# Kernel tuning notes

Hardware: AMD Instinct MI355X
Metric: run time of the kernel (lower is better)

## Reference

```python
import jax, jax.numpy as jnp
import numpy as np

N_EMBD = 1024
N_HEAD = 16
R = 16
SCALING = 1.0 / 16.0  # loralib default lora_alpha=1, scaling = alpha/r


def lora_linear(x, W, b, A, B):
    # loralib: y = x @ W.T + b + (x @ A.T) @ B.T * scaling
    return x @ W.T + b + (x @ A.T) @ B.T * SCALING


def setup_inputs() -> dict:
    key = jax.random.key(0)
    ks = jax.random.split(key, 16)
    B, T, S, C = 8, 1024, 256, N_EMBD
    std = 0.02
    return {
        "x": jax.random.normal(ks[0], (B, T, C), jnp.float32),
        "feature": jax.random.normal(ks[1], (B, S, C), jnp.float32),
        # c_attn (q projection)
        "Wq": jax.random.normal(ks[2], (C, C), jnp.float32) * std,
        "bq": jnp.zeros((C,), jnp.float32),
        "Aq": jax.random.normal(ks[3], (R, C), jnp.float32) * std,
        "Bq": jnp.zeros((C, R), jnp.float32),
        # feature_attn (kv projection)
        "Wf": jax.random.normal(ks[4], (2 * C, C), jnp.float32) * std,
        "bf": jnp.zeros((2 * C,), jnp.float32),
        "Af": jax.random.normal(ks[5], (R, C), jnp.float32) * std,
        "Bf": jnp.zeros((2 * C, R), jnp.float32),
        # c_proj
        "Wp": jax.random.normal(ks[6], (C, C), jnp.float32) * std,
        "bp": jnp.zeros((C,), jnp.float32),
        "Ap": jax.random.normal(ks[7], (R, C), jnp.float32) * std,
        "Bp": jnp.zeros((C, R), jnp.float32),
    }


def reference(x, feature, Wq, bq, Aq, Bq, Wf, bf, Af, Bf, Wp, bp, Ap, Bp):
    Bsz, T, C = x.shape
    S = feature.shape[1]
    H = N_HEAD
    D = C // H

    q = lora_linear(x, Wq, bq, Aq, Bq).reshape(Bsz, T, H, D).transpose(0, 2, 1, 3)
    kv = lora_linear(feature, Wf, bf, Af, Bf)
    k, v = kv[..., :C], kv[..., C:]
    k = k.reshape(Bsz, S, H, D).transpose(0, 2, 1, 3)
    v = v.reshape(Bsz, S, H, D).transpose(0, 2, 1, 3)

    att = jnp.einsum("bhtd,bhsd->bhts", q, k) * (1.0 / np.sqrt(D))
    mask = jnp.tril(jnp.ones((T, S), bool))  # bias[:, :, :T, :S]
    att = jnp.where(mask, att, -jnp.inf)
    att = jax.nn.softmax(att, axis=-1)

    y = jnp.einsum("bhts,bhsd->bhtd", att, v)
    y = y.transpose(0, 2, 1, 3).reshape(Bsz, T, C)
    return lora_linear(y, Wp, bp, Ap, Bp)
```

## Files before the change

### kernel.cpp

```cpp
#include <hip/hip_runtime.h>
#include <hip/hip_bf16.h>
#include <stdint.h>
#include <stddef.h>

typedef __hip_bfloat16 bf16;
typedef __attribute__((ext_vector_type(8))) short short8;
typedef __attribute__((ext_vector_type(4))) float floatx4;

__device__ __forceinline__ void async_load16(const bf16* g, bf16* l) {
#if defined(__has_builtin) && __has_builtin(__builtin_amdgcn_global_load_lds)
  __builtin_amdgcn_global_load_lds((__attribute__((address_space(1))) void*)g,
                                   (__attribute__((address_space(3))) void*)l,
                                   16, 0, 0);
#else
  *(short8*)l = *(const short8*)g;
#endif
}

__device__ __forceinline__ int wave_detect_f32(const unsigned short* __restrict__ xr) {
  const int lane = threadIdx.x & 63;
  const unsigned short u = xr[lane];
  const int e = (u >> 7) & 0xFF;
  const unsigned long long m = __ballot(e >= 0x93);
  return (__popcll(m) > 5) ? 1 : 0;
}

__device__ __forceinline__ float ldf(const void* p, int i, int flg) {
  return flg ? ((const float*)p)[i] : __bfloat162float(((const bf16*)p)[i]);
}

struct PrepArgs {
  const void *x, *ft, *bq, *bf, *bp;
  const void *Wq, *Aq, *Bq, *Wf, *Af, *Bf, *Wp, *Ap, *Bp;
  bf16 *cx, *cft, *cbq, *cbf, *cbp, *weffq, *wefff, *weffp;
};

__device__ __forceinline__ void canon4(const void* src, bf16* dst, int i4, int flg) {
  if (flg) {
    const float4 v = ((const float4*)src)[i4];
    dst[i4 * 4 + 0] = __float2bfloat16(v.x);
    dst[i4 * 4 + 1] = __float2bfloat16(v.y);
    dst[i4 * 4 + 2] = __float2bfloat16(v.z);
    dst[i4 * 4 + 3] = __float2bfloat16(v.w);
  } else {
    ((uint2*)dst)[i4] = ((const uint2*)src)[i4];
  }
}

__device__ __forceinline__ void weff1(const void* W, const void* Bm, const void* Am,
                                      bf16* dst, int idx, int flg) {
  const int n = idx >> 10, k = idx & 1023;
  float acc = 0.f;
#pragma unroll
  for (int r = 0; r < 16; ++r)
    acc += ldf(Bm, n * 16 + r, flg) * ldf(Am, r * 1024 + k, flg);
  dst[idx] = __float2bfloat16(ldf(W, idx, flg) + 0.0625f * acc);
}

__global__ __launch_bounds__(256) void prep_kernel(PrepArgs a) {
  const int flg = wave_detect_f32((const unsigned short*)a.x);
  const int bid = blockIdx.x, tid = threadIdx.x;
  if (bid < 8192) {
    canon4(a.x, a.cx, bid * 256 + tid, flg);
  } else if (bid < 10240) {
    canon4(a.ft, a.cft, (bid - 8192) * 256 + tid, flg);
  } else if (bid < 10241) {
    canon4(a.bq, a.cbq, tid, flg);
  } else if (bid < 10243) {
    canon4(a.bf, a.cbf, (bid - 10241) * 256 + tid, flg);
  } else if (bid < 10244) {
    canon4(a.bp, a.cbp, tid, flg);
  } else if (bid < 14340) {
    weff1(a.Wq, a.Bq, a.Aq, a.weffq, (bid - 10244) * 256 + tid, flg);
  } else if (bid < 22532) {
    weff1(a.Wf, a.Bf, a.Af, a.wefff, (bid - 14340) * 256 + tid, flg);
  } else {
    weff1(a.Wp, a.Bp, a.Ap, a.weffp, (bid - 22532) * 256 + tid, flg);
  }
}

#define SLOT ((128 + 128) * 32)

__device__ __forceinline__ void stage_slot(const bf16* __restrict__ gA,
                                           const bf16* __restrict__ gB,
                                           bf16* slot, int tid) {
#pragma unroll
  for (int l = 0; l < 2; ++l) {
    const int D = l * 256 + tid;
    const int r = D >> 2;
    const int c = (D & 3) ^ ((r >> 1) & 3);
    async_load16(gA + (size_t)r * 1024 + c * 8, slot + D * 8);
  }
#pragma unroll
  for (int l = 0; l < 2; ++l) {
    const int D = l * 256 + tid;
    const int r = D >> 2;
    const int c = (D & 3) ^ ((r >> 1) & 3);
    async_load16(gB + (size_t)r * 1024 + c * 8, slot + 128 * 32 + D * 8);
  }
}

__device__ __forceinline__ void gemm_core(const bf16* __restrict__ A,
                                          const bf16* __restrict__ Bt,
                                          int bm, int bn, bf16* sT,
                                          floatx4 (&acc)[4][4]) {
  const int tid = threadIdx.x;
  const int wave = tid >> 6, lane = tid & 63;
  const int lrow = lane & 15, quad = lane >> 4;
  const int wm64 = (wave >> 1) << 6;
  const int wn64 = (wave & 1) << 6;
  const int pc0 = ((quad ^ ((lrow >> 1) & 3)) << 3);

  const bf16* gA = A + (size_t)bm * 1024;
  const bf16* gB = Bt + (size_t)bn * 1024;

  stage_slot(gA, gB, sT, tid);
  stage_slot(gA + 32, gB + 32, sT + SLOT, tid);

#pragma unroll
  for (int t = 0; t < 32; ++t) {
    asm volatile("s_waitcnt lgkmcnt(0)" ::: "memory");
    __builtin_amdgcn_s_barrier();
    __builtin_amdgcn_sched_barrier(0);
    if (t < 30) {
      stage_slot(gA + (t + 2) * 32, gB + (t + 2) * 32,
                 sT + ((t + 2) % 3) * SLOT, tid);
      asm volatile("s_waitcnt vmcnt(8)" ::: "memory");
    } else if (t == 30) {
      asm volatile("s_waitcnt vmcnt(4)" ::: "memory");
    } else {
      asm volatile("s_waitcnt vmcnt(0)" ::: "memory");
    }
    __builtin_amdgcn_s_barrier();
    __builtin_amdgcn_sched_barrier(0);

    const bf16* slotA = sT + (t % 3) * SLOT;
    const bf16* slotB = slotA + 128 * 32;
    short8 a_[4], b_[4];
#pragma unroll
    for (int i = 0; i < 4; ++i) {
      a_[i] = *(const short8*)(slotA + (wm64 + i * 16 + lrow) * 32 + pc0);
      b_[i] = *(const short8*)(slotB + (wn64 + i * 16 + lrow) * 32 + pc0);
    }
    __builtin_amdgcn_s_setprio(1);
#pragma unroll
    for (int i = 0; i < 4; ++i)
#pragma unroll
      for (int j = 0; j < 4; ++j)
        acc[i][j] = __builtin_amdgcn_mfma_f32_16x16x32_bf16(
            a_[i], b_[j], acc[i][j], 0, 0, 0);
    __builtin_amdgcn_s_setprio(0);
  }
}

__global__ __launch_bounds__(256, 3) void gemm_qkv(
    const bf16* __restrict__ cx, const bf16* __restrict__ cft,
    const bf16* __restrict__ weffq, const bf16* __restrict__ wefff,
    const bf16* __restrict__ cbq, const bf16* __restrict__ cbf,
    bf16* __restrict__ qws, bf16* __restrict__ kws, bf16* __restrict__ vtws) {
  __shared__ __align__(16) bf16 sT[3 * SLOT];
  const int bid = blockIdx.x;
  int mode, bm, bn;
  const bf16 *A, *Bt, *bias;
  if (bid < 512) {
    mode = 0; A = cx; Bt = weffq; bias = cbq;
    bm = (((bid & 7) << 3) | ((bid >> 3) & 7)) * 128;
    bn = (bid >> 6) * 128;
  } else {
    const int b2 = bid - 512;
    mode = 1; A = cft; Bt = wefff; bias = cbf;
    bm = (((b2 & 7) << 1) | ((b2 >> 3) & 1)) * 128;
    bn = (b2 >> 4) * 128;
  }

  const floatx4 zero4 = {0.f, 0.f, 0.f, 0.f};
  floatx4 acc[4][4];
#pragma unroll
  for (int i = 0; i < 4; ++i)
#pragma unroll
    for (int j = 0; j < 4; ++j) acc[i][j] = zero4;

  gemm_core(A, Bt, bm, bn, sT, acc);

  const int tid = threadIdx.x, wave = tid >> 6, lane = tid & 63;
  const int lrow = lane & 15, quad = lane >> 4;
  const int wm64 = (wave >> 1) << 6, wn64 = (wave & 1) << 6;
#pragma unroll
  for (int i = 0; i < 4; ++i) {
    const int mbase = bm + wm64 + i * 16 + quad * 4;
#pragma unroll
    for (int j = 0; j < 4; ++j) {
      const int n = bn + wn64 + j * 16 + lrow;
      const float bv = __bfloat162float(bias[n]);
#pragma unroll
      for (int r = 0; r < 4; ++r) {
        const int m = mbase + r;
        const bf16 hval = __float2bfloat16(acc[i][j][r] + bv);
        if (mode == 0) {
          const int b = m >> 10, t = m & 1023, hh = n >> 6, d = n & 63;
          qws[(((size_t)(b * 16 + hh)) * 1024 + t) * 64 + d] = hval;
        } else {
          const int b = m >> 8, s = m & 255;
          if (n < 1024) {
            const int hh = n >> 6, d = n & 63;
            kws[(((size_t)(b * 16 + hh)) * 256 + s) * 64 + d] = hval;
          } else {
            const int nn = n - 1024, hh = nn >> 6, d = nn & 63;
            vtws[(((size_t)(b * 16 + hh)) * 64 + d) * 256 + s] = hval;
          }
        }
      }
    }
  }
}

__global__ __launch_bounds__(256, 3) void gemm_out(
    const bf16* __restrict__ A, const bf16* __restrict__ Bt,
    const bf16* __restrict__ bias, void* __restrict__ out0,
    const unsigned short* __restrict__ xraw) {
  __shared__ __align__(16) bf16 sT[3 * SLOT];
  const int bid = blockIdx.x;
  const int bm = (((bid & 7) << 3) | ((bid >> 3) & 7)) * 128;
  const int bn = (bid >> 6) * 128;
  const int N = 1024;

  const floatx4 zero4 = {0.f, 0.f, 0.f, 0.f};
  floatx4 acc[4][4];
#pragma unroll
  for (int i = 0; i < 4; ++i)
#pragma unroll
    for (int j = 0; j < 4; ++j) acc[i][j] = zero4;

  gemm_core(A, Bt, bm, bn, sT, acc);

  const int tid = threadIdx.x, wave = tid >> 6, lane = tid & 63;
  const int lrow = lane & 15, quad = lane >> 4;
  const int wm64 = (wave >> 1) << 6, wn64 = (wave & 1) << 6;
  const int flg = wave_detect_f32(xraw);
#pragma unroll
  for (int i = 0; i < 4; ++i) {
    const int mbase = bm + wm64 + i * 16 + quad * 4;
#pragma unroll
    for (int j = 0; j < 4; ++j) {
      const int n = bn + wn64 + j * 16 + lrow;
      const float bv = __bfloat162float(bias[n]);
#pragma unroll
      for (int r = 0; r < 4; ++r) {
        const int m = mbase + r;
        const float fval = acc[i][j][r] + bv;
        const size_t idx = (size_t)m * N + n;
        if (flg) ((float*)out0)[idx] = fval;
        else     ((bf16*)out0)[idx] = __float2bfloat16(fval);
      }
    }
  }
}

#define SKP 72
#define SVP 264
__global__ __launch_bounds__(512, 2) void attn_kernel(
    const bf16* __restrict__ qws, const bf16* __restrict__ kws,
    const bf16* __restrict__ vtws, bf16* __restrict__ yws) {
  const int b = blockIdx.z, h = blockIdx.y, qc = blockIdx.x;
  const int bh = b * 16 + h;
  __shared__ __align__(16) bf16 sK[256 * SKP];
  __shared__ __align__(16) bf16 sVt[64 * SVP];
  __shared__ __align__(16) bf16 sP[8][16 * SVP];
  const int tid = threadIdx.x, wave = tid >> 6, lane = tid & 63;
  const int lrow = lane & 15, quad = lane >> 4;
  const bf16* kg = kws + (size_t)bh * (256 * 64);
  const bf16* vg = vtws + (size_t)bh * (64 * 256);
#pragma unroll
  for (int i = 0; i < 4; ++i) {
    const int idx = i * 512 + tid;
    const int kr = idx >> 3, kc = (idx & 7) * 8;
    *(short8*)(sK + kr * SKP + kc) = *(const short8*)(kg + kr * 64 + kc);
    const int vr = idx >> 5, vc = (idx & 31) * 8;
    *(short8*)(sVt + vr * SVP + vc) = *(const short8*)(vg + vr * 256 + vc);
  }
  __syncthreads();
  bf16* sPw = sP[wave];
  const floatx4 zero4 = {0.f, 0.f, 0.f, 0.f};
  const float kscale = 0.18033688011112042f;

  for (int st = 0; st < 4; ++st) {
    const int t0 = qc * 512 + wave * 64 + st * 16;
    const bf16* qrow = qws + ((size_t)bh * 1024 + t0 + lrow) * 64;
    const short8 aq0 = *(const short8*)(qrow + quad * 8);
    const short8 aq1 = *(const short8*)(qrow + 32 + quad * 8);
    floatx4 sc[16];
#pragma unroll
    for (int nt = 0; nt < 16; ++nt) {
      floatx4 c = zero4;
      c = __builtin_amdgcn_mfma_f32_16x16x32_bf16(
          aq0, *(const short8*)(sK + (nt * 16 + lrow) * SKP + quad * 8), c, 0, 0, 0);
      c = __builtin_amdgcn_mfma_f32_16x16x32_bf16(
          aq1, *(const short8*)(sK + (nt * 16 + lrow) * SKP + 32 + quad * 8), c, 0, 0, 0);
      sc[nt] = c;
    }
    float sum[4] = {0.f, 0.f, 0.f, 0.f};
#pragma unroll
    for (int nt = 0; nt < 16; ++nt) {
      const int s = nt * 16 + lrow;
#pragma unroll
      for (int r = 0; r < 4; ++r) {
        const int t = t0 + quad * 4 + r;
        const float p = (s <= t) ? exp2f(sc[nt][r] * kscale) : 0.f;
        sum[r] += p;
        sPw[(quad * 4 + r) * SVP + nt * 16 + lrow] = __float2bfloat16(p);
      }
    }
#pragma unroll
    for (int r = 0; r < 4; ++r) {
      sum[r] += __shfl_xor(sum[r], 1, 16);
      sum[r] += __shfl_xor(sum[r], 2, 16);
      sum[r] += __shfl_xor(sum[r], 4, 16);
      sum[r] += __shfl_xor(sum[r], 8, 16);
    }
    asm volatile("s_waitcnt lgkmcnt(0)" ::: "memory");
    floatx4 ya[4];
#pragma unroll
    for (int nt = 0; nt < 4; ++nt) ya[nt] = zero4;
#pragma unroll
    for (int ks = 0; ks < 8; ++ks) {
      const short8 ap = *(const short8*)(sPw + lrow * SVP + ks * 32 + quad * 8);
#pragma unroll
      for (int nt = 0; nt < 4; ++nt)
        ya[nt] = __builtin_amdgcn_mfma_f32_16x16x32_bf16(
            ap, *(const short8*)(sVt + (nt * 16 + lrow) * SVP + ks * 32 + quad * 8),
            ya[nt], 0, 0, 0);
    }
#pragma unroll
    for (int r = 0; r < 4; ++r) {
      const float rl = 1.f / sum[r];
      const int t = t0 + quad * 4 + r;
#pragma unroll
      for (int nt = 0; nt < 4; ++nt)
        yws[((size_t)b * 1024 + t) * 1024 + h * 64 + nt * 16 + lrow] =
            __float2bfloat16(ya[nt][r] * rl);
    }
  }
}

extern "C" void kernel_launch(void* const* d_in, const int* in_sizes, int n_in,
                              void* d_out, int out_size, void* d_ws, size_t ws_size,
                              hipStream_t stream) {
  char* p = (char*)d_ws;
  bf16* cbq   = (bf16*)p;     p += 4096;
  bf16* cbf   = (bf16*)p;     p += 8192;
  bf16* cbp   = (bf16*)p;     p += 4096;
  bf16* weffq = (bf16*)p;     p += (size_t)1024 * 1024 * 2;
  bf16* wefff = (bf16*)p;     p += (size_t)2048 * 1024 * 2;
  bf16* weffp = (bf16*)p;     p += (size_t)1024 * 1024 * 2;
  bf16* qws   = (bf16*)p;     p += (size_t)8 * 16 * 1024 * 64 * 2;
  bf16* kws   = (bf16*)p;     p += (size_t)8 * 16 * 256 * 64 * 2;
  bf16* vtws  = (bf16*)p;     p += (size_t)8 * 16 * 64 * 256 * 2;
  bf16* cft   = (bf16*)p;     p += (size_t)8 * 256 * 1024 * 2;
  bf16* cx    = (bf16*)p;     p += (size_t)8 * 1024 * 1024 * 2;
  bf16* yws   = cx;
  const size_t required = (size_t)(p - (char*)d_ws);
  if (ws_size < required) return;

  PrepArgs pa;
  pa.x = d_in[0]; pa.ft = d_in[1];
  pa.bq = d_in[3]; pa.bf = d_in[7]; pa.bp = d_in[11];
  pa.Wq = d_in[2];  pa.Aq = d_in[4];  pa.Bq = d_in[5];
  pa.Wf = d_in[6];  pa.Af = d_in[8];  pa.Bf = d_in[9];
  pa.Wp = d_in[10]; pa.Ap = d_in[12]; pa.Bp = d_in[13];
  pa.cx = cx; pa.cft = cft; pa.cbq = cbq; pa.cbf = cbf; pa.cbp = cbp;
  pa.weffq = weffq; pa.wefff = wefff; pa.weffp = weffp;
  prep_kernel<<<26628, 256, 0, stream>>>(pa);

  gemm_qkv<<<768, 256, 0, stream>>>(cx, cft, weffq, wefff, cbq, cbf, qws, kws, vtws);
  attn_kernel<<<dim3(2, 16, 8), 512, 0, stream>>>(qws, kws, vtws, yws);
  gemm_out<<<512, 256, 0, stream>>>(yws, weffp, cbp, d_out, (const unsigned short*)d_in[0]);
}
```

Measured before the change: 224.7 us.

## Enlarge GEMM tiles to 256-wide with 4-stage pipeline and vectorize prep kernel

```diff
diff --git a/kernel.cpp b/kernel.cpp
--- a/kernel.cpp
+++ b/kernel.cpp
@@ -25,106 +25,137 @@
   return (__popcll(m) > 5) ? 1 : 0;
 }
 
-__device__ __forceinline__ float ldf(const void* p, int i, int flg) {
-  return flg ? ((const float*)p)[i] : __bfloat162float(((const bf16*)p)[i]);
-}
-
 struct PrepArgs {
   const void *x, *ft, *bq, *bf, *bp;
   const void *Wq, *Aq, *Bq, *Wf, *Af, *Bf, *Wp, *Ap, *Bp;
   bf16 *cx, *cft, *cbq, *cbf, *cbp, *weffq, *wefff, *weffp;
 };
 
-__device__ __forceinline__ void canon4(const void* src, bf16* dst, int i4, int flg) {
+__device__ __forceinline__ void canon8(const void* src, bf16* dst, int i8, int flg) {
   if (flg) {
-    const float4 v = ((const float4*)src)[i4];
-    dst[i4 * 4 + 0] = __float2bfloat16(v.x);
-    dst[i4 * 4 + 1] = __float2bfloat16(v.y);
-    dst[i4 * 4 + 2] = __float2bfloat16(v.z);
-    dst[i4 * 4 + 3] = __float2bfloat16(v.w);
+    const float4 v0 = ((const float4*)src)[i8 * 2];
+    const float4 v1 = ((const float4*)src)[i8 * 2 + 1];
+    bf16 o[8];
+    o[0] = __float2bfloat16(v0.x); o[1] = __float2bfloat16(v0.y);
+    o[2] = __float2bfloat16(v0.z); o[3] = __float2bfloat16(v0.w);
+    o[4] = __float2bfloat16(v1.x); o[5] = __float2bfloat16(v1.y);
+    o[6] = __float2bfloat16(v1.z); o[7] = __float2bfloat16(v1.w);
+    *(uint4*)(dst + i8 * 8) = *(const uint4*)o;
   } else {
-    ((uint2*)dst)[i4] = ((const uint2*)src)[i4];
-  }
-}
-
-__device__ __forceinline__ void weff1(const void* W, const void* Bm, const void* Am,
-                                      bf16* dst, int idx, int flg) {
-  const int n = idx >> 10, k = idx & 1023;
-  float acc = 0.f;
-#pragma unroll
-  for (int r = 0; r < 16; ++r)
-    acc += ldf(Bm, n * 16 + r, flg) * ldf(Am, r * 1024 + k, flg);
-  dst[idx] = __float2bfloat16(ldf(W, idx, flg) + 0.0625f * acc);
+    ((uint4*)dst)[i8] = ((const uint4*)src)[i8];
+  }
+}
+
+__device__ __forceinline__ void weff4(const void* W, const void* Bm, const void* Am,
+                                      bf16* dst, int idx4, int flg) {
+  const int n = idx4 >> 8, k = (idx4 & 255) << 2;
+  float a0 = 0.f, a1 = 0.f, a2 = 0.f, a3 = 0.f;
+  float w0, w1, w2, w3;
+  if (flg) {
+    const float* Af = (const float*)Am;
+    const float* Bf = (const float*)Bm;
+#pragma unroll
+    for (int r = 0; r < 16; ++r) {
+      const float4 av = *(const float4*)(Af + r * 1024 + k);
+      const float bv = Bf[n * 16 + r];
+      a0 += bv * av.x; a1 += bv * av.y; a2 += bv * av.z; a3 += bv * av.w;
+    }
+    const float4 wv = *(const float4*)((const float*)W + n * 1024 + k);
+    w0 = wv.x; w1 = wv.y; w2 = wv.z; w3 = wv.w;
+  } else {
+    const bf16* Ab = (const bf16*)Am;
+    const bf16* Bb = (const bf16*)Bm;
+#pragma unroll
+    for (int r = 0; r < 16; ++r) {
+      const float bv = __bfloat162float(Bb[n * 16 + r]);
+      const bf16* ap = Ab + r * 1024 + k;
+      a0 += bv * __bfloat162float(ap[0]);
+      a1 += bv * __bfloat162float(ap[1]);
+      a2 += bv * __bfloat162float(ap[2]);
+      a3 += bv * __bfloat162float(ap[3]);
+    }
+    const bf16* Wb = (const bf16*)W + n * 1024 + k;
+    w0 = __bfloat162float(Wb[0]); w1 = __bfloat162float(Wb[1]);
+    w2 = __bfloat162float(Wb[2]); w3 = __bfloat162float(Wb[3]);
+  }
+  bf16 o[4];
+  o[0] = __float2bfloat16(w0 + 0.0625f * a0);
+  o[1] = __float2bfloat16(w1 + 0.0625f * a1);
+  o[2] = __float2bfloat16(w2 + 0.0625f * a2);
+  o[3] = __float2bfloat16(w3 + 0.0625f * a3);
+  *(uint2*)(dst + idx4 * 4) = *(const uint2*)o;
 }
 
 __global__ __launch_bounds__(256) void prep_kernel(PrepArgs a) {
   const int flg = wave_detect_f32((const unsigned short*)a.x);
   const int bid = blockIdx.x, tid = threadIdx.x;
-  if (bid < 8192) {
-    canon4(a.x, a.cx, bid * 256 + tid, flg);
-  } else if (bid < 10240) {
-    canon4(a.ft, a.cft, (bid - 8192) * 256 + tid, flg);
-  } else if (bid < 10241) {
-    canon4(a.bq, a.cbq, tid, flg);
-  } else if (bid < 10243) {
-    canon4(a.bf, a.cbf, (bid - 10241) * 256 + tid, flg);
-  } else if (bid < 10244) {
-    canon4(a.bp, a.cbp, tid, flg);
-  } else if (bid < 14340) {
-    weff1(a.Wq, a.Bq, a.Aq, a.weffq, (bid - 10244) * 256 + tid, flg);
-  } else if (bid < 22532) {
-    weff1(a.Wf, a.Bf, a.Af, a.wefff, (bid - 14340) * 256 + tid, flg);
+  if (bid < 4096) {
+    canon8(a.x, a.cx, bid * 256 + tid, flg);
+  } else if (bid < 5120) {
+    canon8(a.ft, a.cft, (bid - 4096) * 256 + tid, flg);
+  } else if (bid < 5122) {
+    const int e8 = (bid - 5120) * 256 + tid;
+    if (e8 < 128) canon8(a.bq, a.cbq, e8, flg);
+    else if (e8 < 384) canon8(a.bf, a.cbf, e8 - 128, flg);
+    else canon8(a.bp, a.cbp, e8 - 384, flg);
+  } else if (bid < 6146) {
+    weff4(a.Wq, a.Bq, a.Aq, a.weffq, (bid - 5122) * 256 + tid, flg);
+  } else if (bid < 8194) {
+    weff4(a.Wf, a.Bf, a.Af, a.wefff, (bid - 6146) * 256 + tid, flg);
   } else {
-    weff1(a.Wp, a.Bp, a.Ap, a.weffp, (bid - 22532) * 256 + tid, flg);
-  }
-}
-
-#define SLOT ((128 + 128) * 32)
-
-__device__ __forceinline__ void stage_slot(const bf16* __restrict__ gA,
-                                           const bf16* __restrict__ gB,
-                                           bf16* slot, int tid) {
+    weff4(a.Wp, a.Bp, a.Ap, a.weffp, (bid - 8194) * 256 + tid, flg);
+  }
+}
+
+#define QSLOT (256 * 32)
+#define RSLOT (2 * QSLOT)
+
+__device__ __forceinline__ void stage256(const bf16* __restrict__ gA,
+                                         const bf16* __restrict__ gB,
+                                         bf16* slot, int tid) {
 #pragma unroll
   for (int l = 0; l < 2; ++l) {
-    const int D = l * 256 + tid;
+    const int D = l * 512 + tid;
     const int r = D >> 2;
     const int c = (D & 3) ^ ((r >> 1) & 3);
     async_load16(gA + (size_t)r * 1024 + c * 8, slot + D * 8);
   }
 #pragma unroll
   for (int l = 0; l < 2; ++l) {
-    const int D = l * 256 + tid;
+    const int D = l * 512 + tid;
     const int r = D >> 2;
     const int c = (D & 3) ^ ((r >> 1) & 3);
-    async_load16(gB + (size_t)r * 1024 + c * 8, slot + 128 * 32 + D * 8);
-  }
-}
-
-__device__ __forceinline__ void gemm_core(const bf16* __restrict__ A,
-                                          const bf16* __restrict__ Bt,
-                                          int bm, int bn, bf16* sT,
-                                          floatx4 (&acc)[4][4]) {
+    async_load16(gB + (size_t)r * 1024 + c * 8, slot + QSLOT + D * 8);
+  }
+}
+
+__device__ __forceinline__ void gemm_core256(const bf16* __restrict__ A,
+                                             const bf16* __restrict__ Bt,
+                                             int bm, int bn, bf16* sT,
+                                             floatx4 (&acc)[8][4]) {
   const int tid = threadIdx.x;
   const int wave = tid >> 6, lane = tid & 63;
   const int lrow = lane & 15, quad = lane >> 4;
-  const int wm64 = (wave >> 1) << 6;
-  const int wn64 = (wave & 1) << 6;
+  const int wm = (wave >> 2) << 7;
+  const int wn = (wave & 3) << 6;
   const int pc0 = ((quad ^ ((lrow >> 1) & 3)) << 3);
 
   const bf16* gA = A + (size_t)bm * 1024;
   const bf16* gB = Bt + (size_t)bn * 1024;
 
-  stage_slot(gA, gB, sT, tid);
-  stage_slot(gA + 32, gB + 32, sT + SLOT, tid);
-
-#pragma unroll
+  stage256(gA,      gB,      sT,             tid);
+  stage256(gA + 32, gB + 32, sT + RSLOT,     tid);
+  stage256(gA + 64, gB + 64, sT + 2 * RSLOT, tid);
+
+#pragma unroll 4
   for (int t = 0; t < 32; ++t) {
     asm volatile("s_waitcnt lgkmcnt(0)" ::: "memory");
     __builtin_amdgcn_s_barrier();
     __builtin_amdgcn_sched_barrier(0);
-    if (t < 30) {
-      stage_slot(gA + (t + 2) * 32, gB + (t + 2) * 32,
-                 sT + ((t + 2) % 3) * SLOT, tid);
+    if (t < 29) {
+      stage256(gA + (t + 3) * 32, gB + (t + 3) * 32, sT + ((t + 3) & 3) * RSLOT, tid);
+      asm volatile("s_waitcnt vmcnt(12)" ::: "memory");
+    } else if (t == 29) {
       asm volatile("s_waitcnt vmcnt(8)" ::: "memory");
     } else if (t == 30) {
       asm volatile("s_waitcnt vmcnt(4)" ::: "memory");
@@ -134,17 +165,18 @@
     __builtin_amdgcn_s_barrier();
     __builtin_amdgcn_sched_barrier(0);
 
-    const bf16* slotA = sT + (t % 3) * SLOT;
-    const bf16* slotB = slotA + 128 * 32;
-    short8 a_[4], b_[4];
-#pragma unroll
-    for (int i = 0; i < 4; ++i) {
-      a_[i] = *(const short8*)(slotA + (wm64 + i * 16 + lrow) * 32 + pc0);
-      b_[i] = *(const short8*)(slotB + (wn64 + i * 16 + lrow) * 32 + pc0);
-    }
+    const bf16* slotA = sT + (t & 3) * RSLOT;
+    const bf16* slotB = slotA + QSLOT;
+    short8 a_[8], b_[4];
+#pragma unroll
+    for (int i = 0; i < 8; ++i)
+      a_[i] = *(const short8*)(slotA + (wm + i * 16 + lrow) * 32 + pc0);
+#pragma unroll
+    for (int j = 0; j < 4; ++j)
+      b_[j] = *(const short8*)(slotB + (wn + j * 16 + lrow) * 32 + pc0);
     __builtin_amdgcn_s_setprio(1);
 #pragma unroll
-    for (int i = 0; i < 4; ++i)
+    for (int i = 0; i < 8; ++i)
 #pragma unroll
       for (int j = 0; j < 4; ++j)
         acc[i][j] = __builtin_amdgcn_mfma_f32_16x16x32_bf16(
@@ -153,44 +185,119 @@
   }
 }
 
-__global__ __launch_bounds__(256, 3) void gemm_qkv(
+#define QSLOTB (128 * 32)
+#define RSLOTO (QSLOT + QSLOTB)
+
+__device__ __forceinline__ void stage128(const bf16* __restrict__ gA,
+                                         const bf16* __restrict__ gB,
+                                         bf16* slot, int tid) {
+#pragma unroll
+  for (int l = 0; l < 2; ++l) {
+    const int D = l * 512 + tid;
+    const int r = D >> 2;
+    const int c = (D & 3) ^ ((r >> 1) & 3);
+    async_load16(gA + (size_t)r * 1024 + c * 8, slot + D * 8);
+  }
+  {
+    const int D = tid;
+    const int r = D >> 2;
+    const int c = (D & 3) ^ ((r >> 1) & 3);
+    async_load16(gB + (size_t)r * 1024 + c * 8, slot + QSLOT + D * 8);
+  }
+}
+
+__device__ __forceinline__ void gemm_core128(const bf16* __restrict__ A,
+                                             const bf16* __restrict__ Bt,
+                                             int bm, int bn, bf16* sT,
+                                             floatx4 (&acc)[4][4]) {
+  const int tid = threadIdx.x;
+  const int wave = tid >> 6, lane = tid & 63;
+  const int lrow = lane & 15, quad = lane >> 4;
+  const int wm = (wave >> 1) << 6;
+  const int wn = (wave & 1) << 6;
+  const int pc0 = ((quad ^ ((lrow >> 1) & 3)) << 3);
+
+  const bf16* gA = A + (size_t)bm * 1024;
+  const bf16* gB = Bt + (size_t)bn * 1024;
+
+  stage128(gA,      gB,      sT,             tid);
+  stage128(gA + 32, gB + 32, sT + RSLOTO,     tid);
+  stage128(gA + 64, gB + 64, sT + 2 * RSLOTO, tid);
+
+#pragma unroll 4
+  for (int t = 0; t < 32; ++t) {
+    asm volatile("s_waitcnt lgkmcnt(0)" ::: "memory");
+    __builtin_amdgcn_s_barrier();
+    __builtin_amdgcn_sched_barrier(0);
+    if (t < 29) {
+      stage128(gA + (t + 3) * 32, gB + (t + 3) * 32, sT + ((t + 3) & 3) * RSLOTO, tid);
+      asm volatile("s_waitcnt vmcnt(9)" ::: "memory");
+    } else if (t == 29) {
+      asm volatile("s_waitcnt vmcnt(6)" ::: "memory");
+    } else if (t == 30) {
+      asm volatile("s_waitcnt vmcnt(3)" ::: "memory");
+    } else {
+      asm volatile("s_waitcnt vmcnt(0)" ::: "memory");
+    }
+    __builtin_amdgcn_s_barrier();
+    __builtin_amdgcn_sched_barrier(0);
+
+    const bf16* slotA = sT + (t & 3) * RSLOTO;
+    const bf16* slotB = slotA + QSLOT;
+    short8 a_[4], b_[4];
+#pragma unroll
+    for (int i = 0; i < 4; ++i) {
+      a_[i] = *(const short8*)(slotA + (wm + i * 16 + lrow) * 32 + pc0);
+      b_[i] = *(const short8*)(slotB + (wn + i * 16 + lrow) * 32 + pc0);
+    }
+    __builtin_amdgcn_s_setprio(1);
+#pragma unroll
+    for (int i = 0; i < 4; ++i)
+#pragma unroll
+      for (int j = 0; j < 4; ++j)
+        acc[i][j] = __builtin_amdgcn_mfma_f32_16x16x32_bf16(
+            a_[i], b_[j], acc[i][j], 0, 0, 0);
+    __builtin_amdgcn_s_setprio(0);
+  }
+}
+
+__global__ __launch_bounds__(512, 1) void gemm_qkv(
     const bf16* __restrict__ cx, const bf16* __restrict__ cft,
     const bf16* __restrict__ weffq, const bf16* __restrict__ wefff,
     const bf16* __restrict__ cbq, const bf16* __restrict__ cbf,
     bf16* __restrict__ qws, bf16* __restrict__ kws, bf16* __restrict__ vtws) {
-  __shared__ __align__(16) bf16 sT[3 * SLOT];
+  __shared__ __align__(16) bf16 sT[4 * RSLOT];
   const int bid = blockIdx.x;
+  const int swz = (bid & 7) * 24 + (bid >> 3);
   int mode, bm, bn;
   const bf16 *A, *Bt, *bias;
-  if (bid < 512) {
+  if (swz < 128) {
     mode = 0; A = cx; Bt = weffq; bias = cbq;
-    bm = (((bid & 7) << 3) | ((bid >> 3) & 7)) * 128;
-    bn = (bid >> 6) * 128;
+    bm = (swz >> 2) * 256; bn = (swz & 3) * 256;
   } else {
-    const int b2 = bid - 512;
+    const int s2 = swz - 128;
     mode = 1; A = cft; Bt = wefff; bias = cbf;
-    bm = (((b2 & 7) << 1) | ((b2 >> 3) & 1)) * 128;
-    bn = (b2 >> 4) * 128;
+    bm = (s2 >> 3) * 256; bn = (s2 & 7) * 256;
   }
 
   const floatx4 zero4 = {0.f, 0.f, 0.f, 0.f};
-  floatx4 acc[4][4];
-#pragma unroll
-  for (int i = 0; i < 4; ++i)
+  floatx4 acc[8][4];
+#pragma unroll
+  for (int i = 0; i < 8; ++i)
 #pragma unroll
     for (int j = 0; j < 4; ++j) acc[i][j] = zero4;
 
-  gemm_core(A, Bt, bm, bn, sT, acc);
+  gemm_core256(A, Bt, bm, bn, sT, acc);
 
   const int tid = threadIdx.x, wave = tid >> 6, lane = tid & 63;
   const int lrow = lane & 15, quad = lane >> 4;
-  const int wm64 = (wave >> 1) << 6, wn64 = (wave & 1) << 6;
-#pragma unroll
-  for (int i = 0; i < 4; ++i) {
-    const int mbase = bm + wm64 + i * 16 + quad * 4;
+  const int wm = (wave >> 2) << 7, wn = (wave & 3) << 6;
+#pragma unroll
+  for (int i = 0; i < 8; ++i) {
+    const int mbase = bm + wm + i * 16 + quad * 4;
 #pragma unroll
     for (int j = 0; j < 4; ++j) {
-      const int n = bn + wn64 + j * 16 + lrow;
+      const int n = bn + wn + j * 16 + lrow;
       const float bv = __bfloat162float(bias[n]);
 #pragma unroll
       for (int r = 0; r < 4; ++r) {
@@ -214,14 +321,14 @@
   }
 }
 
-__global__ __launch_bounds__(256, 3) void gemm_out(
+__global__ __launch_bounds__(512, 1) void gemm_out(
     const bf16* __restrict__ A, const bf16* __restrict__ Bt,
     const bf16* __restrict__ bias, void* __restrict__ out0,
     const unsigned short* __restrict__ xraw) {
-  __shared__ __align__(16) bf16 sT[3 * SLOT];
+  __shared__ __align__(16) bf16 sT[4 * RSLOTO];
   const int bid = blockIdx.x;
-  const int bm = (((bid & 7) << 3) | ((bid >> 3) & 7)) * 128;
-  const int bn = (bid >> 6) * 128;
+  const int swz = (bid & 7) * 32 + (bid >> 3);
+  const int bm = (swz >> 3) * 256, bn = (swz & 7) * 128;
   const int N = 1024;
 
   const floatx4 zero4 = {0.f, 0.f, 0.f, 0.f};
@@ -231,18 +338,18 @@
 #pragma unroll
     for (int j = 0; j < 4; ++j) acc[i][j] = zero4;
 
-  gemm_core(A, Bt, bm, bn, sT, acc);
+  gemm_core128(A, Bt, bm, bn, sT, acc);
 
   const int tid = threadIdx.x, wave = tid >> 6, lane = tid & 63;
   const int lrow = lane & 15, quad = lane >> 4;
-  const int wm64 = (wave >> 1) << 6, wn64 = (wave & 1) << 6;
+  const int wm = (wave >> 1) << 6, wn = (wave & 1) << 6;
   const int flg = wave_detect_f32(xraw);
 #pragma unroll
   for (int i = 0; i < 4; ++i) {
-    const int mbase = bm + wm64 + i * 16 + quad * 4;
+    const int mbase = bm + wm + i * 16 + quad * 4;
 #pragma unroll
     for (int j = 0; j < 4; ++j) {
-      const int n = bn + wn64 + j * 16 + lrow;
+      const int n = bn + wn + j * 16 + lrow;
       const float bv = __bfloat162float(bias[n]);
 #pragma unroll
       for (int r = 0; r < 4; ++r) {
@@ -369,9 +476,9 @@
   pa.Wp = d_in[10]; pa.Ap = d_in[12]; pa.Bp = d_in[13];
   pa.cx = cx; pa.cft = cft; pa.cbq = cbq; pa.cbf = cbf; pa.cbp = cbp;
   pa.weffq = weffq; pa.wefff = wefff; pa.weffp = weffp;
-  prep_kernel<<<26628, 256, 0, stream>>>(pa);
-
-  gemm_qkv<<<768, 256, 0, stream>>>(cx, cft, weffq, wefff, cbq, cbf, qws, kws, vtws);
+  prep_kernel<<<9218, 256, 0, stream>>>(pa);
+
+  gemm_qkv<<<192, 512, 0, stream>>>(cx, cft, weffq, wefff, cbq, cbf, qws, kws, vtws);
   attn_kernel<<<dim3(2, 16, 8), 512, 0, stream>>>(qws, kws, vtws, yws);
-  gemm_out<<<512, 256, 0, stream>>>(yws, weffp, cbp, d_out, (const unsigned short*)d_in[0]);
-}
+  gemm_out<<<256, 512, 0, stream>>>(yws, weffp, cbp, d_out, (const unsigned short*)d_in[0]);
+}
```

New measurement: 239.2 us. +6.5%, slower.
